# Optimization experiments

Hardware: AMD Instinct MI355X
Metric: run time of the kernel (lower is better)

The kernel has to match this reference:

```python
import jax, jax.numpy as jnp
import numpy as np

EMBED = 1024
HEADS = 16
HEAD_DIM = EMBED // HEADS


def setup_inputs() -> dict:
    key = jax.random.key(0)
    ks = jax.random.split(key, 9)
    s = 0.02
    return {
        "hidden_states": jax.random.normal(ks[0], (1, 4, 1500, EMBED), dtype=jnp.float32),
        "q_w": jax.random.normal(ks[1], (EMBED, EMBED), dtype=jnp.float32) * s,
        "q_b": jax.random.normal(ks[2], (EMBED,), dtype=jnp.float32) * s,
        "k_w": jax.random.normal(ks[3], (EMBED, EMBED), dtype=jnp.float32) * s,
        "v_w": jax.random.normal(ks[4], (EMBED, EMBED), dtype=jnp.float32) * s,
        "v_b": jax.random.normal(ks[5], (EMBED,), dtype=jnp.float32) * s,
        "out_w": jax.random.normal(ks[6], (EMBED, EMBED), dtype=jnp.float32) * s,
        "out_b": jax.random.normal(ks[7], (EMBED,), dtype=jnp.float32) * s,
    }


def reference(hidden_states, q_w, q_b, k_w, v_w, v_b, out_w, out_b):
    # hidden_states: [1, B, S, E]
    _, bsz, tgt_len, _ = hidden_states.shape
    x = hidden_states[0]  # [B, S, E]
    scaling = HEAD_DIM ** -0.5

    def split_heads(t):  # [B, S, E] -> [B, H, S, Dh]
        return t.reshape(bsz, tgt_len, HEADS, HEAD_DIM).transpose(0, 2, 1, 3)

    # Linear layers use torch convention: y = x @ W.T + b  (k_proj has no bias)
    q = split_heads((x @ q_w.T + q_b) * scaling)
    k = split_heads(x @ k_w.T)
    v = split_heads(x @ v_w.T + v_b)

    # attention scores [B, H, S, S]
    attn_weights = jnp.einsum("bhqd,bhkd->bhqk", q, k)
    attn_probs = jax.nn.softmax(attn_weights, axis=-1)
    attn_out = jnp.einsum("bhqk,bhkd->bhqd", attn_probs, v)  # [B, H, S, Dh]

    attn_out = attn_out.transpose(0, 2, 1, 3).reshape(1, bsz, tgt_len, EMBED)
    return attn_out @ out_w.T + out_b
```

## Files before the change

### kernel.cpp

```cpp
#include <hip/hip_runtime.h>
#include <cstddef>
#include <cstdint>

#define EMB 1024
#define SEQ 1500
#define NB 4
#define NH 16
#define DH 64
#define MTOT (NB*SEQ)
#define VTS 1536

typedef __bf16 bf16;
typedef __bf16 bf16x4 __attribute__((ext_vector_type(4)));
typedef __bf16 bf16x8 __attribute__((ext_vector_type(8)));
typedef short  s16x4  __attribute__((ext_vector_type(4)));
typedef float  f32x4  __attribute__((ext_vector_type(4)));

__device__ __forceinline__ void async16(const void* g, const void* l) {
    __builtin_amdgcn_global_load_lds(
        (const __attribute__((address_space(1))) uint32_t*)g,
        (__attribute__((address_space(3))) uint32_t*)l, 16, 0, 0);
}

struct CvtArgs {
    const float* src[5];
    bf16* dst[5];
    int n[5];
};

__global__ __launch_bounds__(256) void cvt_kernel(CvtArgs a) {
    const int s = blockIdx.y;
    const float* __restrict__ src = a.src[s];
    bf16* __restrict__ dst = a.dst[s];
    const int n = a.n[s];
    for (int i = (blockIdx.x * 256 + threadIdx.x) * 4; i < n; i += gridDim.x * 1024) {
        float4 v = *(const float4*)(src + i);
        bf16x4 o = { (bf16)v.x, (bf16)v.y, (bf16)v.z, (bf16)v.w };
        *(bf16x4*)(dst + i) = o;
    }
}

__global__ __launch_bounds__(256) void gemm_fused(
    const bf16* __restrict__ X,
    const bf16* __restrict__ W0, const bf16* __restrict__ W1, const bf16* __restrict__ W2,
    const float* __restrict__ b_q, const float* __restrict__ b_v, const float* __restrict__ b_o,
    bf16* __restrict__ Oq, bf16* __restrict__ Ok, bf16* __restrict__ Ovt,
    float* __restrict__ Of, int M, int qkv)
{
    __shared__ bf16 As[128 * 32];
    __shared__ bf16 Bs[128 * 32];
    const int tid = threadIdx.x;
    const int lane = tid & 63, w = tid >> 6;
    const int q = lane >> 4, lr = lane & 15;
    const int wr = w >> 1, wc = w & 1;
    const int m0 = blockIdx.x * 128;

    int proj, n0;
    if (qkv) { proj = blockIdx.y >> 3; n0 = (blockIdx.y & 7) * 128; }
    else     { proj = 3;               n0 = blockIdx.y * 128; }

    const bf16 *PA, *PB;
    int baseA, baseB, limA, limB;
    if (proj == 2) {
        PA = X;  baseA = m0; limA = M;
        PB = W2; baseB = n0; limB = EMB;
    } else {
        PA = (proj == 0) ? W0 : (proj == 1 ? W1 : W0);
        baseA = n0; limA = EMB;
        PB = X; baseB = m0; limB = M;
    }

    f32x4 acc[4][4] = {};
    const int srow = w * 32 + (lane >> 2);
    const int kchk = (lane & 3) * 8;

    for (int k0 = 0; k0 < EMB; k0 += 32) {
        __syncthreads();
#pragma unroll
        for (int i = 0; i < 2; i++) {
            int ar = srow + i * 16;
            int ra = baseA + ar; ra = ra < limA ? ra : limA - 1;
            int rb = baseB + ar; rb = rb < limB ? rb : limB - 1;
            async16(PA + (size_t)ra * EMB + k0 + kchk, As + (w * 2 + i) * 512);
            async16(PB + (size_t)rb * EMB + k0 + kchk, Bs + (w * 2 + i) * 512);
        }
        __syncthreads();

        bf16x8 af[4], bfr[4];
#pragma unroll
        for (int t = 0; t < 4; t++) {
            af[t]  = *(const bf16x8*)(As + (wr * 64 + t * 16 + lr) * 32 + q * 8);
            bfr[t] = *(const bf16x8*)(Bs + (wc * 64 + t * 16 + lr) * 32 + q * 8);
        }
#pragma unroll
        for (int ti = 0; ti < 4; ti++)
#pragma unroll
            for (int tj = 0; tj < 4; tj++)
                acc[ti][tj] = __builtin_amdgcn_mfma_f32_16x16x32_bf16(
                    af[ti], bfr[tj], acc[ti][tj], 0, 0, 0);
    }

    if (proj <= 1) {
        const float scale = (proj == 0) ? 0.125f : 1.0f;
        const float* bias = (proj == 0) ? b_q : nullptr;
        bf16* O = (proj == 0) ? Oq : Ok;
#pragma unroll
        for (int tj = 0; tj < 4; tj++) {
            const int m = m0 + wc * 64 + tj * 16 + lr;
            if (m >= M) continue;
            const int b_ = m / SEQ, s_ = m % SEQ;
#pragma unroll
            for (int ti = 0; ti < 4; ti++) {
                const int nb = n0 + wr * 64 + ti * 16 + q * 4;
                const int h = nb >> 6, d = nb & 63;
                float4 b4 = bias ? *(const float4*)(bias + nb)
                                 : make_float4(0.f, 0.f, 0.f, 0.f);
                bf16x4 o;
                o[0] = (bf16)((acc[ti][tj][0] + b4.x) * scale);
                o[1] = (bf16)((acc[ti][tj][1] + b4.y) * scale);
                o[2] = (bf16)((acc[ti][tj][2] + b4.z) * scale);
                o[3] = (bf16)((acc[ti][tj][3] + b4.w) * scale);
                *(bf16x4*)(O + (((size_t)b_ * NH + h) * SEQ + s_) * DH + d) = o;
            }
        }
    } else if (proj == 2) {
#pragma unroll
        for (int ti = 0; ti < 4; ti++) {
            const int mb = m0 + wr * 64 + ti * 16 + q * 4;
            if (mb >= M) continue;
            const int b_ = mb / SEQ, s_ = mb % SEQ;
#pragma unroll
            for (int tj = 0; tj < 4; tj++) {
                const int nb = n0 + wc * 64 + tj * 16 + lr;
                const int h = nb >> 6, d = nb & 63;
                const float bv = b_v[nb];
                bf16x4 o;
                o[0] = (bf16)(acc[ti][tj][0] + bv);
                o[1] = (bf16)(acc[ti][tj][1] + bv);
                o[2] = (bf16)(acc[ti][tj][2] + bv);
                o[3] = (bf16)(acc[ti][tj][3] + bv);
                *(bf16x4*)(Ovt + ((size_t)(b_ * NH + h) * DH + d) * VTS + s_) = o;
            }
        }
    } else {
#pragma unroll
        for (int tj = 0; tj < 4; tj++) {
            const int m = m0 + wc * 64 + tj * 16 + lr;
            if (m >= M) continue;
#pragma unroll
            for (int ti = 0; ti < 4; ti++) {
                const int nb = n0 + wr * 64 + ti * 16 + q * 4;
                const float4 b4 = *(const float4*)(b_o + nb);
                float4 o;
                o.x = acc[ti][tj][0] + b4.x;
                o.y = acc[ti][tj][1] + b4.y;
                o.z = acc[ti][tj][2] + b4.z;
                o.w = acc[ti][tj][3] + b4.w;
                *(float4*)(Of + (size_t)m * EMB + nb) = o;
            }
        }
    }
}

__global__ __launch_bounds__(256) void attn_mfma(
    const bf16* __restrict__ Qb, const bf16* __restrict__ Kb,
    const bf16* __restrict__ Vt, bf16* __restrict__ ctx)
{
    __shared__ bf16 Ks[64][72];
    __shared__ bf16 Vs[64][72];
    const int tid = threadIdx.x;
    const int lane = tid & 63, w = tid >> 6;
    const int q = lane >> 4, lr = lane & 15;
    const int bh = blockIdx.x, b_ = bh >> 4, h_ = bh & 15;
    const int q0 = blockIdx.y * 128;
    const size_t base = (size_t)bh * SEQ * DH;
    const size_t vbase = (size_t)bh * DH * VTS;

    int qrow[2];
    bf16x8 qf[2][2];
#pragma unroll
    for (int g = 0; g < 2; g++) {
        qrow[g] = q0 + g * 64 + w * 16 + lr;
        const int qrc = qrow[g] < SEQ ? qrow[g] : (SEQ - 1);
        qf[g][0] = *(const bf16x8*)(Qb + base + (size_t)qrc * DH + q * 8);
        qf[g][1] = *(const bf16x8*)(Qb + base + (size_t)qrc * DH + 32 + q * 8);
    }

    f32x4 oacc[2][4] = {};
    float lsum[2] = {0.f, 0.f};

    const int srow = tid >> 3;
    const int sch  = (tid & 7) * 8;

    const int NT = (SEQ + 63) / 64;
    for (int kt = 0; kt < NT; kt++) {
        const int k0 = kt * 64;
        int g0 = k0 + srow;      g0 = g0 < SEQ ? g0 : (SEQ - 1);
        int g1 = k0 + 32 + srow; g1 = g1 < SEQ ? g1 : (SEQ - 1);
        const uint4 ka = *(const uint4*)(Kb + base + (size_t)g0 * DH + sch);
        const uint4 kb = *(const uint4*)(Kb + base + (size_t)g1 * DH + sch);
        const uint4 va = *(const uint4*)(Vt + vbase + (size_t)srow * VTS + k0 + sch);
        const uint4 vb = *(const uint4*)(Vt + vbase + (size_t)(srow + 32) * VTS + k0 + sch);
        __syncthreads();
        *(uint4*)&Ks[srow][sch]      = ka;
        *(uint4*)&Ks[srow + 32][sch] = kb;
        *(uint4*)&Vs[srow][sch]      = va;
        *(uint4*)&Vs[srow + 32][sch] = vb;
        __syncthreads();

        bf16x8 kf[2][4];
#pragma unroll
        for (int s = 0; s < 2; s++)
#pragma unroll
            for (int mt = 0; mt < 4; mt++)
                kf[s][mt] = *(const bf16x8*)(&Ks[mt * 16 + lr][s * 32 + q * 8]);

        s16x4 pf[2][4];
#pragma unroll
        for (int g = 0; g < 2; g++) {
            f32x4 st[4] = {};
#pragma unroll
            for (int s = 0; s < 2; s++)
#pragma unroll
                for (int mt = 0; mt < 4; mt++)
                    st[mt] = __builtin_amdgcn_mfma_f32_16x16x32_bf16(
                        kf[s][mt], qf[g][s], st[mt], 0, 0, 0);

            if (k0 + 64 > SEQ) {
#pragma unroll
                for (int mt = 0; mt < 4; mt++)
#pragma unroll
                    for (int r = 0; r < 4; r++)
                        if (k0 + mt * 16 + q * 4 + r >= SEQ) st[mt][r] = -1e30f;
            }

            float ps = lsum[g];
#pragma unroll
            for (int mt = 0; mt < 4; mt++) {
                bf16x4 pb;
#pragma unroll
                for (int r = 0; r < 4; r++) {
                    const float p = __expf(st[mt][r]);
                    ps += p;
                    pb[r] = (bf16)p;
                }
                pf[g][mt] = __builtin_bit_cast(s16x4, pb);
            }
            lsum[g] = ps;
        }

#pragma unroll
        for (int c = 0; c < 4; c++) {
#pragma unroll
            for (int dt = 0; dt < 4; dt++) {
                const s16x4 vf = __builtin_bit_cast(s16x4,
                    *(const bf16x4*)(&Vs[dt * 16 + lr][c * 16 + q * 4]));
                oacc[0][dt] = __builtin_amdgcn_mfma_f32_16x16x16bf16_1k(
                    vf, pf[0][c], oacc[0][dt], 0, 0, 0);
                oacc[1][dt] = __builtin_amdgcn_mfma_f32_16x16x16bf16_1k(
                    vf, pf[1][c], oacc[1][dt], 0, 0, 0);
            }
        }
    }

#pragma unroll
    for (int g = 0; g < 2; g++) {
        float l = lsum[g];
        l += __shfl_xor(l, 16, 64);
        l += __shfl_xor(l, 32, 64);
        const float inv = 1.0f / l;
        if (qrow[g] < SEQ) {
            const size_t rowoff = ((size_t)b_ * SEQ + qrow[g]) * EMB + h_ * DH;
#pragma unroll
            for (int dt = 0; dt < 4; dt++) {
                bf16x4 o;
#pragma unroll
                for (int r = 0; r < 4; r++) o[r] = (bf16)(oacc[g][dt][r] * inv);
                *(bf16x4*)(ctx + rowoff + dt * 16 + q * 4) = o;
            }
        }
    }
}

extern "C" void kernel_launch(void* const* d_in, const int* in_sizes, int n_in,
                              void* d_out, int out_size, void* d_ws, size_t ws_size,
                              hipStream_t stream) {
    const float* x     = (const float*)d_in[0];
    const float* q_w   = (const float*)d_in[1];
    const float* q_b   = (const float*)d_in[2];
    const float* k_w   = (const float*)d_in[3];
    const float* v_w   = (const float*)d_in[4];
    const float* v_b   = (const float*)d_in[5];
    const float* out_w = (const float*)d_in[6];
    const float* out_b = (const float*)d_in[7];
    float* out = (float*)d_out;

    const size_t nbuf = (size_t)MTOT * EMB;
    const size_t nvt  = (size_t)NB * NH * DH * VTS;
    const size_t nw   = (size_t)EMB * EMB;
    bf16* xb  = (bf16*)d_ws;
    bf16* qws = xb  + nbuf;
    bf16* kws = qws + nbuf;
    bf16* vtw = kws + nbuf;
    bf16* wqb = vtw + nvt;
    bf16* wkb = wqb + nw;
    bf16* wvb = wkb + nw;
    bf16* wob = wvb + nw;
    bf16* ctx = xb;

    CvtArgs ca;
    ca.src[0] = x;     ca.dst[0] = xb;  ca.n[0] = (int)nbuf;
    ca.src[1] = q_w;   ca.dst[1] = wqb; ca.n[1] = (int)nw;
    ca.src[2] = k_w;   ca.dst[2] = wkb; ca.n[2] = (int)nw;
    ca.src[3] = v_w;   ca.dst[3] = wvb; ca.n[3] = (int)nw;
    ca.src[4] = out_w; ca.dst[4] = wob; ca.n[4] = (int)nw;
    cvt_kernel<<<dim3(1024, 5), 256, 0, stream>>>(ca);

    gemm_fused<<<dim3((MTOT + 127) / 128, 24), 256, 0, stream>>>(
        xb, wqb, wkb, wvb, q_b, v_b, nullptr, qws, kws, vtw, nullptr, MTOT, 1);

    attn_mfma<<<dim3(NB * NH, (SEQ + 127) / 128), 256, 0, stream>>>(qws, kws, vtw, ctx);

    gemm_fused<<<dim3((MTOT + 127) / 128, 8), 256, 0, stream>>>(
        ctx, wob, nullptr, nullptr, nullptr, nullptr, out_b,
        nullptr, nullptr, nullptr, out, MTOT, 0);
}
```

Before: 259.6 us.

## Double-buffer GEMM LDS tiles, prefetch attention K/V, fold log2e into Q scale

```diff
diff --git a/kernel.cpp b/kernel.cpp
--- a/kernel.cpp
+++ b/kernel.cpp
@@ -16,6 +16,8 @@
 typedef short  s16x4  __attribute__((ext_vector_type(4)));
 typedef float  f32x4  __attribute__((ext_vector_type(4)));
 
+#define LOG2E 1.44269504088896340736f
+
 __device__ __forceinline__ void async16(const void* g, const void* l) {
     __builtin_amdgcn_global_load_lds(
         (const __attribute__((address_space(1))) uint32_t*)g,
@@ -23,20 +25,27 @@
 }
 
 struct CvtArgs {
-    const float* src[5];
-    bf16* dst[5];
-    int n[5];
+    const float* xs; bf16* xd;
+    const float* w[4]; bf16* wd[4];
 };
 
 __global__ __launch_bounds__(256) void cvt_kernel(CvtArgs a) {
-    const int s = blockIdx.y;
-    const float* __restrict__ src = a.src[s];
-    bf16* __restrict__ dst = a.dst[s];
-    const int n = a.n[s];
-    for (int i = (blockIdx.x * 256 + threadIdx.x) * 4; i < n; i += gridDim.x * 1024) {
-        float4 v = *(const float4*)(src + i);
+    const size_t NX = (size_t)MTOT * EMB;
+    const size_t NW = (size_t)EMB * EMB;
+    const size_t tot = NX + 4 * NW;
+    for (size_t i = ((size_t)blockIdx.x * 256 + threadIdx.x) * 4; i < tot;
+         i += (size_t)gridDim.x * 1024) {
+        const float* s; bf16* d; size_t off;
+        if (i < NX) { s = a.xs; d = a.xd; off = i; }
+        else {
+            size_t j = i - NX;
+            int wi = (int)(j >> 20);
+            off = j & (NW - 1);
+            s = a.w[wi]; d = a.wd[wi];
+        }
+        float4 v = *(const float4*)(s + off);
         bf16x4 o = { (bf16)v.x, (bf16)v.y, (bf16)v.z, (bf16)v.w };
-        *(bf16x4*)(dst + i) = o;
+        *(bf16x4*)(d + off) = o;
     }
 }
 
@@ -47,17 +56,22 @@
     bf16* __restrict__ Oq, bf16* __restrict__ Ok, bf16* __restrict__ Ovt,
     float* __restrict__ Of, int M, int qkv)
 {
-    __shared__ bf16 As[128 * 32];
-    __shared__ bf16 Bs[128 * 32];
+    __shared__ bf16 As[2][128 * 32];
+    __shared__ bf16 Bs[2][128 * 32];
     const int tid = threadIdx.x;
     const int lane = tid & 63, w = tid >> 6;
     const int q = lane >> 4, lr = lane & 15;
     const int wr = w >> 1, wc = w & 1;
-    const int m0 = blockIdx.x * 128;
+
+    const int id = blockIdx.x;
+    const int t_ = id >> 3;
+    const int mtile = (id & 7) + (t_ % 6) * 8;
+    const int y = t_ / 6;
+    const int m0 = mtile * 128;
 
     int proj, n0;
-    if (qkv) { proj = blockIdx.y >> 3; n0 = (blockIdx.y & 7) * 128; }
-    else     { proj = 3;               n0 = blockIdx.y * 128; }
+    if (qkv) { proj = y >> 3; n0 = (y & 7) * 128; }
+    else     { proj = 3;      n0 = y * 128; }
 
     const bf16 *PA, *PB;
     int baseA, baseB, limA, limB;
@@ -71,26 +85,46 @@
     }
 
     f32x4 acc[4][4] = {};
+
     const int srow = w * 32 + (lane >> 2);
-    const int kchk = (lane & 3) * 8;
+    const int swz_ch = (((lane & 3) ^ ((lane >> 3) & 3))) * 8;
+    const bf16* pA[2]; const bf16* pB[2];
+#pragma unroll
+    for (int i = 0; i < 2; i++) {
+        int ra = baseA + srow + i * 16; ra = ra < limA ? ra : limA - 1;
+        int rb = baseB + srow + i * 16; rb = rb < limB ? rb : limB - 1;
+        pA[i] = PA + (size_t)ra * EMB + swz_ch;
+        pB[i] = PB + (size_t)rb * EMB + swz_ch;
+    }
+
+#pragma unroll
+    for (int i = 0; i < 2; i++) {
+        async16(pA[i], As[0] + (w * 2 + i) * 512);
+        async16(pB[i], Bs[0] + (w * 2 + i) * 512);
+    }
+
+    const int qsw = (q ^ ((lr >> 1) & 3)) * 8;
+    const int arow = (wr * 64 + lr) * 32;
+    const int brow = (wc * 64 + lr) * 32;
 
     for (int k0 = 0; k0 < EMB; k0 += 32) {
+        const int cur = (k0 >> 5) & 1;
         __syncthreads();
-#pragma unroll
-        for (int i = 0; i < 2; i++) {
-            int ar = srow + i * 16;
-            int ra = baseA + ar; ra = ra < limA ? ra : limA - 1;
-            int rb = baseB + ar; rb = rb < limB ? rb : limB - 1;
-            async16(PA + (size_t)ra * EMB + k0 + kchk, As + (w * 2 + i) * 512);
-            async16(PB + (size_t)rb * EMB + k0 + kchk, Bs + (w * 2 + i) * 512);
-        }
-        __syncthreads();
-
+        const int nxt = k0 + 32;
+        if (nxt < EMB) {
+#pragma unroll
+            for (int i = 0; i < 2; i++) {
+                async16(pA[i] + nxt, As[cur ^ 1] + (w * 2 + i) * 512);
+                async16(pB[i] + nxt, Bs[cur ^ 1] + (w * 2 + i) * 512);
+            }
+        }
+        const bf16* Ab = As[cur];
+        const bf16* Bb = Bs[cur];
         bf16x8 af[4], bfr[4];
 #pragma unroll
         for (int t = 0; t < 4; t++) {
-            af[t]  = *(const bf16x8*)(As + (wr * 64 + t * 16 + lr) * 32 + q * 8);
-            bfr[t] = *(const bf16x8*)(Bs + (wc * 64 + t * 16 + lr) * 32 + q * 8);
+            af[t]  = *(const bf16x8*)(Ab + arow + t * 512 + qsw);
+            bfr[t] = *(const bf16x8*)(Bb + brow + t * 512 + qsw);
         }
 #pragma unroll
         for (int ti = 0; ti < 4; ti++)
@@ -101,7 +135,7 @@
     }
 
     if (proj <= 1) {
-        const float scale = (proj == 0) ? 0.125f : 1.0f;
+        const float scale = (proj == 0) ? 0.125f * LOG2E : 1.0f;
         const float* bias = (proj == 0) ? b_q : nullptr;
         bf16* O = (proj == 0) ? Oq : Ok;
 #pragma unroll
@@ -193,14 +227,19 @@
     const int sch  = (tid & 7) * 8;
 
     const int NT = (SEQ + 63) / 64;
+
+    uint4 ka, kb, va, vb;
+    {
+        int g0 = srow;
+        int g1 = 32 + srow;
+        ka = *(const uint4*)(Kb + base + (size_t)g0 * DH + sch);
+        kb = *(const uint4*)(Kb + base + (size_t)g1 * DH + sch);
+        va = *(const uint4*)(Vt + vbase + (size_t)srow * VTS + sch);
+        vb = *(const uint4*)(Vt + vbase + (size_t)(srow + 32) * VTS + sch);
+    }
+
     for (int kt = 0; kt < NT; kt++) {
         const int k0 = kt * 64;
-        int g0 = k0 + srow;      g0 = g0 < SEQ ? g0 : (SEQ - 1);
-        int g1 = k0 + 32 + srow; g1 = g1 < SEQ ? g1 : (SEQ - 1);
-        const uint4 ka = *(const uint4*)(Kb + base + (size_t)g0 * DH + sch);
-        const uint4 kb = *(const uint4*)(Kb + base + (size_t)g1 * DH + sch);
-        const uint4 va = *(const uint4*)(Vt + vbase + (size_t)srow * VTS + k0 + sch);
-        const uint4 vb = *(const uint4*)(Vt + vbase + (size_t)(srow + 32) * VTS + k0 + sch);
         __syncthreads();
         *(uint4*)&Ks[srow][sch]      = ka;
         *(uint4*)&Ks[srow + 32][sch] = kb;
@@ -208,6 +247,16 @@
         *(uint4*)&Vs[srow + 32][sch] = vb;
         __syncthreads();
 
+        if (kt + 1 < NT) {
+            const int n0_ = k0 + 64;
+            int g0 = n0_ + srow;      g0 = g0 < SEQ ? g0 : (SEQ - 1);
+            int g1 = n0_ + 32 + srow; g1 = g1 < SEQ ? g1 : (SEQ - 1);
+            ka = *(const uint4*)(Kb + base + (size_t)g0 * DH + sch);
+            kb = *(const uint4*)(Kb + base + (size_t)g1 * DH + sch);
+            va = *(const uint4*)(Vt + vbase + (size_t)srow * VTS + n0_ + sch);
+            vb = *(const uint4*)(Vt + vbase + (size_t)(srow + 32) * VTS + n0_ + sch);
+        }
+
         bf16x8 kf[2][4];
 #pragma unroll
         for (int s = 0; s < 2; s++)
@@ -240,7 +289,7 @@
                 bf16x4 pb;
 #pragma unroll
                 for (int r = 0; r < 4; r++) {
-                    const float p = __expf(st[mt][r]);
+                    const float p = exp2f(st[mt][r]);
                     ps += p;
                     pb[r] = (bf16)p;
                 }
@@ -309,19 +358,19 @@
     bf16* ctx = xb;
 
     CvtArgs ca;
-    ca.src[0] = x;     ca.dst[0] = xb;  ca.n[0] = (int)nbuf;
-    ca.src[1] = q_w;   ca.dst[1] = wqb; ca.n[1] = (int)nw;
-    ca.src[2] = k_w;   ca.dst[2] = wkb; ca.n[2] = (int)nw;
-    ca.src[3] = v_w;   ca.dst[3] = wvb; ca.n[3] = (int)nw;
-    ca.src[4] = out_w; ca.dst[4] = wob; ca.n[4] = (int)nw;
-    cvt_kernel<<<dim3(1024, 5), 256, 0, stream>>>(ca);
-
-    gemm_fused<<<dim3((MTOT + 127) / 128, 24), 256, 0, stream>>>(
+    ca.xs = x;      ca.xd = xb;
+    ca.w[0] = q_w;  ca.wd[0] = wqb;
+    ca.w[1] = k_w;  ca.wd[1] = wkb;
+    ca.w[2] = v_w;  ca.wd[2] = wvb;
+    ca.w[3] = out_w; ca.wd[3] = wob;
+    cvt_kernel<<<dim3(2560), 256, 0, stream>>>(ca);
+
+    gemm_fused<<<dim3(48 * 24), 256, 0, stream>>>(
         xb, wqb, wkb, wvb, q_b, v_b, nullptr, qws, kws, vtw, nullptr, MTOT, 1);
 
     attn_mfma<<<dim3(NB * NH, (SEQ + 127) / 128), 256, 0, stream>>>(qws, kws, vtw, ctx);
 
-    gemm_fused<<<dim3((MTOT + 127) / 128, 8), 256, 0, stream>>>(
+    gemm_fused<<<dim3(48 * 8), 256, 0, stream>>>(
         ctx, wob, nullptr, nullptr, nullptr, nullptr, out_b,
         nullptr, nullptr, nullptr, out, MTOT, 0);
 }
```

Result: no change. 260.9 us (+0.5%).
